# Optimization experiments

Measured on AMD Instinct MI355X. Metric: run time of the kernel, lower is better.

Reference implementation:

```python
import jax, jax.numpy as jnp
import numpy as np

N_NODES = 100000
HIDDEN = 128
N_LAYERS = 3
N_EDGES = 600000


def setup_inputs() -> dict:
    key = jax.random.key(0)
    k_e, k_emb, k_w = jax.random.split(key, 3)
    edge_index = jax.random.randint(k_e, (2, N_EDGES), 0, N_NODES, dtype=jnp.int64 if jax.config.read('jax_enable_x64') else jnp.int32)
    embedding = jax.random.normal(k_emb, (N_NODES, HIDDEN), dtype=jnp.float32)
    Ws = jax.random.normal(k_w, (N_LAYERS, HIDDEN, HIDDEN), dtype=jnp.float32) * (1.0 / np.sqrt(HIDDEN))
    bs = jnp.zeros((N_LAYERS, HIDDEN), dtype=jnp.float32)
    return {"edge_index": edge_index, "embedding": embedding, "Ws": Ws, "bs": bs}


def _gcn_forward(embedding, Ws, bs, edge_index):
    N = embedding.shape[0]
    # PyG GCNConv default: add self-loops, symmetric deg^{-1/2} normalization
    loop = jnp.arange(N, dtype=edge_index.dtype)
    src = jnp.concatenate([edge_index[0], loop])  # [E+N]
    dst = jnp.concatenate([edge_index[1], loop])
    deg = jax.ops.segment_sum(jnp.ones_like(dst, dtype=embedding.dtype), dst, num_segments=N)
    dinv = jnp.where(deg > 0, jax.lax.rsqrt(jnp.where(deg > 0, deg, 1.0)), 0.0)
    norm = dinv[src] * dinv[dst]  # [E+N]

    x = embedding
    for l in range(Ws.shape[0]):
        h = x @ Ws[l]                              # [N, d] linear transform
        msg = h[src] * norm[:, None]               # gather + scale
        x = jax.ops.segment_sum(msg, dst, num_segments=N) + bs[l]  # scatter-add
        x = jax.nn.relu(x)
        # dropout is identity in eval mode
    return x


def reference(edge_index, embedding, Ws, bs):
    return _gcn_forward(embedding, Ws, bs, edge_index)
```

## Files before the change

### kernel.cpp

```cpp
#include <hip/hip_runtime.h>
#include <hip/hip_bf16.h>


#define HID 128


__global__ void k_init_cnt(int* cnt, int n) {
    int i = blockIdx.x * blockDim.x + threadIdx.x;
    if (i < n) cnt[i] = 1;
}

__global__ void k_count_edges(const int* __restrict__ ei, int* cnt, int E) {
    int e = blockIdx.x * blockDim.x + threadIdx.x;
    if (e < E) atomicAdd(&cnt[ei[E + e]], 1);
}

__global__ void k_scanA(const int* __restrict__ cnt, int* csum, int n) {
    __shared__ int sd[256];
    int t = threadIdx.x;
    int base = blockIdx.x * 1024 + t * 4;
    int s = 0;
#pragma unroll
    for (int j = 0; j < 4; j++) { int i = base + j; if (i < n) s += cnt[i]; }
    sd[t] = s; __syncthreads();
    for (int off = 128; off > 0; off >>= 1) {
        if (t < off) sd[t] += sd[t + off];
        __syncthreads();
    }
    if (t == 0) csum[blockIdx.x] = sd[0];
}

__global__ void k_scanB(int* csum, int* offsets, int nchunk, int n) {
    __shared__ int sd[256];
    int t = threadIdx.x;
    int v = (t < nchunk) ? csum[t] : 0;
    sd[t] = v; __syncthreads();
    for (int off = 1; off < 256; off <<= 1) {
        int u = (t >= off) ? sd[t - off] : 0;
        __syncthreads();
        sd[t] += u;
        __syncthreads();
    }
    if (t < nchunk) csum[t] = sd[t] - v;
    if (t == 0) offsets[n] = sd[255];
}

__global__ void k_scanC(const int* __restrict__ cnt, const int* __restrict__ csum,
                        int* offsets, int* cursor, float* dinv,
                        int* adj_src, float* adj_norm, int n) {
    __shared__ int sd[256];
    int t = threadIdx.x;
    int base = blockIdx.x * 1024 + t * 4;
    int c[4]; int s = 0;
#pragma unroll
    for (int j = 0; j < 4; j++) {
        c[j] = (base + j < n) ? cnt[base + j] : 0;
        s += c[j];
    }
    sd[t] = s; __syncthreads();
    for (int off = 1; off < 256; off <<= 1) {
        int v = (t >= off) ? sd[t - off] : 0;
        __syncthreads();
        sd[t] += v;
        __syncthreads();
    }
    int run = sd[t] - s + csum[blockIdx.x];
#pragma unroll
    for (int j = 0; j < 4; j++) {
        int i = base + j;
        if (i < n) {
            offsets[i] = run;
            float di = rsqrtf((float)c[j]);
            dinv[i] = di;
            cursor[i] = run + 1;
            adj_src[run] = i;
            adj_norm[run] = di * di;
        }
        run += c[j];
    }
}

__global__ void k_fill_edges(const int* __restrict__ ei, int* cursor,
                             const float* __restrict__ dinv,
                             int* adj_src, float* adj_norm, int E) {
    int e = blockIdx.x * blockDim.x + threadIdx.x;
    if (e >= E) return;
    int s = ei[e];
    int d = ei[E + e];
    int pos = atomicAdd(&cursor[d], 1);
    adj_src[pos] = s;
    adj_norm[pos] = dinv[s] * dinv[d];
}


__global__ __launch_bounds__(256) void k_agg(const float* __restrict__ x,
                                             const int* __restrict__ offsets,
                                             const int* __restrict__ adj_src,
                                             const float* __restrict__ adj_norm,
                                             float* __restrict__ out, int n) {
    int gid = blockIdx.x * blockDim.x + threadIdx.x;
    int node = gid >> 6;
    int lane = gid & 63;
    if (node >= n) return;
    int beg = offsets[node];
    int end = offsets[node + 1];
    int q    = lane >> 4;
    int ql   = lane & 15;
    int f4   = (q & 1) * 16 + ql;
    int epar = q >> 1;
    float4 acc = {0.f, 0.f, 0.f, 0.f};
#pragma unroll 2
    for (int e = beg; e < end; e += 2) {
        int me = e + epar;
        int mc = me < end ? me : end - 1;
        int s  = adj_src[mc];
        float w = me < end ? adj_norm[mc] : 0.f;
        float4 v = ((const float4*)(x + (size_t)s * HID))[f4];
        acc.x += w * v.x;
        acc.y += w * v.y;
        acc.z += w * v.z;
        acc.w += w * v.w;
    }
    acc.x += __shfl_xor(acc.x, 32);
    acc.y += __shfl_xor(acc.y, 32);
    acc.z += __shfl_xor(acc.z, 32);
    acc.w += __shfl_xor(acc.w, 32);
    if (lane < 32)
        ((float4*)(out + (size_t)node * HID))[lane] = acc;
}


__global__ __launch_bounds__(256, 2) void k_gemm_bias_relu(const float* __restrict__ A,
                                                           const float* __restrict__ W,
                                                           const float* __restrict__ bias,
                                                           float* __restrict__ out,
                                                           int nrows) {
    __shared__ float Wl[HID * HID];
    __shared__ float Xs[32 * HID];
    int t = threadIdx.x;

    {
        const float4* Wg = (const float4*)W;
        float4* Wd = (float4*)Wl;
        for (int i = t; i < (HID * HID) / 4; i += 256) Wd[i] = Wg[i];
    }

    int tx = t & 31;
    int ty = t >> 5;
    int ntiles = nrows / 32;

    for (int tile = blockIdx.x; tile < ntiles; tile += gridDim.x) {
        __syncthreads();
        const float4* Ag = (const float4*)(A + (size_t)tile * 32 * HID);
        float4* Xd = (float4*)Xs;
#pragma unroll
        for (int i = 0; i < 4; i++) Xd[t + i * 256] = Ag[t + i * 256];
        __syncthreads();

        float acc[4][4] = {};
#pragma unroll 8
        for (int k = 0; k < HID; k++) {
            float4 wv = ((const float4*)(Wl + k * HID))[tx];
#pragma unroll
            for (int r = 0; r < 4; r++) {
                float xr = Xs[(ty * 4 + r) * HID + k];
                acc[r][0] += xr * wv.x;
                acc[r][1] += xr * wv.y;
                acc[r][2] += xr * wv.z;
                acc[r][3] += xr * wv.w;
            }
        }

        float4 bb = ((const float4*)bias)[tx];
#pragma unroll
        for (int r = 0; r < 4; r++) {
            float4 v;
            v.x = fmaxf(acc[r][0] + bb.x, 0.f);
            v.y = fmaxf(acc[r][1] + bb.y, 0.f);
            v.z = fmaxf(acc[r][2] + bb.z, 0.f);
            v.w = fmaxf(acc[r][3] + bb.w, 0.f);
            ((float4*)(out + (size_t)(tile * 32 + ty * 4 + r) * HID))[tx] = v;
        }
    }
}


extern "C" void kernel_launch(void* const* d_in, const int* in_sizes, int n_in,
                              void* d_out, int out_size, void* d_ws, size_t ws_size,
                              hipStream_t stream) {
    const int* ei = (const int*)d_in[0];
    const float* emb = (const float*)d_in[1];
    const float* Ws = (const float*)d_in[2];
    const float* bs = (const float*)d_in[3];

    const int E = in_sizes[0] / 2;
    const int N = in_sizes[1] / HID;
    const int NL = in_sizes[3] / HID;
    const int TOT = E + N;

    char* p = (char*)d_ws;
    auto carve = [&](size_t bytes) {
        char* r = p;
        p += (bytes + 255) & ~(size_t)255;
        return (void*)r;
    };
    int*   cnt      = (int*)  carve((size_t)N * 4);
    int*   offsets  = (int*)  carve((size_t)(N + 1) * 4);
    int*   cursor   = (int*)  carve((size_t)N * 4);
    float* dinv     = (float*)carve((size_t)N * 4);
    int*   csum     = (int*)  carve(1024 * 4);
    int*   adj_src  = (int*)  carve((size_t)TOT * 4);
    float* adj_norm = (float*)carve((size_t)TOT * 4);
    float* aggbuf   = (float*)carve((size_t)N * HID * 4);
    float* xbuf     = (float*)d_out;

    const int NCHUNK = (N + 1023) / 1024;

    k_init_cnt<<<(N + 255) / 256, 256, 0, stream>>>(cnt, N);
    k_count_edges<<<(E + 255) / 256, 256, 0, stream>>>(ei, cnt, E);
    k_scanA<<<NCHUNK, 256, 0, stream>>>(cnt, csum, N);
    k_scanB<<<1, 256, 0, stream>>>(csum, offsets, NCHUNK, N);
    k_scanC<<<NCHUNK, 256, 0, stream>>>(cnt, csum, offsets, cursor, dinv,
                                        adj_src, adj_norm, N);
    k_fill_edges<<<(E + 255) / 256, 256, 0, stream>>>(ei, cursor, dinv,
                                                      adj_src, adj_norm, E);

    const int aggBlocks = (N * 64 + 255) / 256;
    const float* x = emb;
    for (int l = 0; l < NL; l++) {
        k_agg<<<aggBlocks, 256, 0, stream>>>(x, offsets, adj_src, adj_norm, aggbuf, N);
        k_gemm_bias_relu<<<512, 256, 0, stream>>>(aggbuf, Ws + (size_t)l * HID * HID,
                                                  bs + (size_t)l * HID, xbuf, N);
        x = xbuf;
    }
}
```

Measured before the change: 502.5 us.

## Fuse neighbor aggregation with GEMM+bias+ReLU into one per-layer kernel

Each 512-thread block now gathers and normalizes the neighbor features for a 32-node tile directly into shared memory, then multiplies that tile by the LDS-resident weight matrix and applies bias and ReLU. This replaces the separate aggregation and GEMM kernels per layer and removes the full N×128 intermediate buffer write and re-read. Layer outputs ping-pong between a workspace buffer and the output. The trade-off is that the latency-bound gather now runs at the limited occupancy of a large-LDS persistent block, with the GEMM phase serialized behind it inside each block.

```diff
diff --git a/kernel.cpp b/kernel.cpp
--- a/kernel.cpp
+++ b/kernel.cpp
@@ -93,94 +93,83 @@
 }
 
 
-__global__ __launch_bounds__(256) void k_agg(const float* __restrict__ x,
-                                             const int* __restrict__ offsets,
-                                             const int* __restrict__ adj_src,
-                                             const float* __restrict__ adj_norm,
-                                             float* __restrict__ out, int n) {
-    int gid = blockIdx.x * blockDim.x + threadIdx.x;
-    int node = gid >> 6;
-    int lane = gid & 63;
-    if (node >= n) return;
-    int beg = offsets[node];
-    int end = offsets[node + 1];
+__global__ __launch_bounds__(512, 2) void k_layer(const float* __restrict__ x,
+                                                  const int* __restrict__ offsets,
+                                                  const int* __restrict__ adj_src,
+                                                  const float* __restrict__ adj_norm,
+                                                  const float* __restrict__ W,
+                                                  const float* __restrict__ bias,
+                                                  float* __restrict__ out, int n) {
+    __shared__ float Wl[HID * HID];
+    __shared__ float Xs[32 * HID];
+    int t = threadIdx.x;
+
+    {
+        const float4* Wg = (const float4*)W;
+        float4* Wd = (float4*)Wl;
+#pragma unroll
+        for (int i = 0; i < 8; i++) Wd[t + i * 512] = Wg[t + i * 512];
+    }
+
+    int wave = t >> 6;
+    int lane = t & 63;
     int q    = lane >> 4;
     int ql   = lane & 15;
     int f4   = (q & 1) * 16 + ql;
     int epar = q >> 1;
-    float4 acc = {0.f, 0.f, 0.f, 0.f};
-#pragma unroll 2
-    for (int e = beg; e < end; e += 2) {
-        int me = e + epar;
-        int mc = me < end ? me : end - 1;
-        int s  = adj_src[mc];
-        float w = me < end ? adj_norm[mc] : 0.f;
-        float4 v = ((const float4*)(x + (size_t)s * HID))[f4];
-        acc.x += w * v.x;
-        acc.y += w * v.y;
-        acc.z += w * v.z;
-        acc.w += w * v.w;
-    }
-    acc.x += __shfl_xor(acc.x, 32);
-    acc.y += __shfl_xor(acc.y, 32);
-    acc.z += __shfl_xor(acc.z, 32);
-    acc.w += __shfl_xor(acc.w, 32);
-    if (lane < 32)
-        ((float4*)(out + (size_t)node * HID))[lane] = acc;
-}
-
-
-__global__ __launch_bounds__(256, 2) void k_gemm_bias_relu(const float* __restrict__ A,
-                                                           const float* __restrict__ W,
-                                                           const float* __restrict__ bias,
-                                                           float* __restrict__ out,
-                                                           int nrows) {
-    __shared__ float Wl[HID * HID];
-    __shared__ float Xs[32 * HID];
-    int t = threadIdx.x;
-
-    {
-        const float4* Wg = (const float4*)W;
-        float4* Wd = (float4*)Wl;
-        for (int i = t; i < (HID * HID) / 4; i += 256) Wd[i] = Wg[i];
-    }
-
     int tx = t & 31;
     int ty = t >> 5;
-    int ntiles = nrows / 32;
+    int ntiles = n / 32;
 
     for (int tile = blockIdx.x; tile < ntiles; tile += gridDim.x) {
         __syncthreads();
-        const float4* Ag = (const float4*)(A + (size_t)tile * 32 * HID);
-        float4* Xd = (float4*)Xs;
-#pragma unroll
-        for (int i = 0; i < 4; i++) Xd[t + i * 256] = Ag[t + i * 256];
-        __syncthreads();
-
-        float acc[4][4] = {};
+
+        for (int i = 0; i < 4; i++) {
+            int r = wave * 4 + i;
+            int node = tile * 32 + r;
+            int beg = offsets[node];
+            int end = offsets[node + 1];
+            float4 acc = {0.f, 0.f, 0.f, 0.f};
+#pragma unroll 2
+            for (int e = beg; e < end; e += 2) {
+                int me = e + epar;
+                int mc = me < end ? me : end - 1;
+                int s  = adj_src[mc];
+                float w = me < end ? adj_norm[mc] : 0.f;
+                float4 v = ((const float4*)(x + (size_t)s * HID))[f4];
+                acc.x += w * v.x;
+                acc.y += w * v.y;
+                acc.z += w * v.z;
+                acc.w += w * v.w;
+            }
+            acc.x += __shfl_xor(acc.x, 32);
+            acc.y += __shfl_xor(acc.y, 32);
+            acc.z += __shfl_xor(acc.z, 32);
+            acc.w += __shfl_xor(acc.w, 32);
+            if (lane < 32)
+                ((float4*)(Xs + r * HID))[lane] = acc;
+        }
+        __syncthreads();
+
+        float a00 = 0.f, a01 = 0.f, a02 = 0.f, a03 = 0.f;
+        float a10 = 0.f, a11 = 0.f, a12 = 0.f, a13 = 0.f;
 #pragma unroll 8
         for (int k = 0; k < HID; k++) {
             float4 wv = ((const float4*)(Wl + k * HID))[tx];
-#pragma unroll
-            for (int r = 0; r < 4; r++) {
-                float xr = Xs[(ty * 4 + r) * HID + k];
-                acc[r][0] += xr * wv.x;
-                acc[r][1] += xr * wv.y;
-                acc[r][2] += xr * wv.z;
-                acc[r][3] += xr * wv.w;
-            }
+            float x0 = Xs[(ty * 2) * HID + k];
+            float x1 = Xs[(ty * 2 + 1) * HID + k];
+            a00 += x0 * wv.x; a01 += x0 * wv.y; a02 += x0 * wv.z; a03 += x0 * wv.w;
+            a10 += x1 * wv.x; a11 += x1 * wv.y; a12 += x1 * wv.z; a13 += x1 * wv.w;
         }
-
         float4 bb = ((const float4*)bias)[tx];
-#pragma unroll
-        for (int r = 0; r < 4; r++) {
-            float4 v;
-            v.x = fmaxf(acc[r][0] + bb.x, 0.f);
-            v.y = fmaxf(acc[r][1] + bb.y, 0.f);
-            v.z = fmaxf(acc[r][2] + bb.z, 0.f);
-            v.w = fmaxf(acc[r][3] + bb.w, 0.f);
-            ((float4*)(out + (size_t)(tile * 32 + ty * 4 + r) * HID))[tx] = v;
-        }
+        float4 o0, o1;
+        o0.x = fmaxf(a00 + bb.x, 0.f); o0.y = fmaxf(a01 + bb.y, 0.f);
+        o0.z = fmaxf(a02 + bb.z, 0.f); o0.w = fmaxf(a03 + bb.w, 0.f);
+        o1.x = fmaxf(a10 + bb.x, 0.f); o1.y = fmaxf(a11 + bb.y, 0.f);
+        o1.z = fmaxf(a12 + bb.z, 0.f); o1.w = fmaxf(a13 + bb.w, 0.f);
+        size_t row0 = (size_t)tile * 32 + ty * 2;
+        ((float4*)(out + row0 * HID))[tx] = o0;
+        ((float4*)(out + (row0 + 1) * HID))[tx] = o1;
     }
 }
 
@@ -211,8 +200,8 @@
     int*   csum     = (int*)  carve(1024 * 4);
     int*   adj_src  = (int*)  carve((size_t)TOT * 4);
     float* adj_norm = (float*)carve((size_t)TOT * 4);
-    float* aggbuf   = (float*)carve((size_t)N * HID * 4);
-    float* xbuf     = (float*)d_out;
+    float* xbufA    = (float*)carve((size_t)N * HID * 4);
+    float* xbufB    = (float*)d_out;
 
     const int NCHUNK = (N + 1023) / 1024;
 
@@ -225,12 +214,12 @@
     k_fill_edges<<<(E + 255) / 256, 256, 0, stream>>>(ei, cursor, dinv,
                                                       adj_src, adj_norm, E);
 
-    const int aggBlocks = (N * 64 + 255) / 256;
     const float* x = emb;
     for (int l = 0; l < NL; l++) {
-        k_agg<<<aggBlocks, 256, 0, stream>>>(x, offsets, adj_src, adj_norm, aggbuf, N);
-        k_gemm_bias_relu<<<512, 256, 0, stream>>>(aggbuf, Ws + (size_t)l * HID * HID,
-                                                  bs + (size_t)l * HID, xbuf, N);
-        x = xbuf;
-    }
-}
+        float* o = (l % 2 == 0) ? xbufB : xbufA;
+        k_layer<<<512, 512, 0, stream>>>(x, offsets, adj_src, adj_norm,
+                                         Ws + (size_t)l * HID * HID,
+                                         bs + (size_t)l * HID, o, N);
+        x = o;
+    }
+}
```

New measurement: 496.8 us. Within noise of the previous version (-1.2%).

## Use split-bf16 MFMA GEMM with agg emitting hi/lo bf16 pairs

Applied to the files above, without the earlier changes.

Replaces the scalar FP32 LDS-tiled GEMM with a matrix-core GEMM built on the bf16 16x16x32 MFMA. Both operands are split into hi and lo bf16 parts and combined with three MFMAs to approximate fp32 accuracy. The aggregation kernel now writes the hi/lo bf16 split directly, and a new kernel pre-packs the transposed weights into hi/lo form. This adds extra MFMA work and bf16 conversion cost. Accuracy is near fp32 but not exact, and the B fragments are read straight from global memory rather than LDS.

```diff
diff --git a/kernel.cpp b/kernel.cpp
--- a/kernel.cpp
+++ b/kernel.cpp
@@ -3,6 +3,9 @@
 
 
 #define HID 128
+
+typedef __attribute__((ext_vector_type(8))) short short8;
+typedef __attribute__((ext_vector_type(4))) float floatx4;
 
 
 __global__ void k_init_cnt(int* cnt, int n) {
@@ -92,12 +95,28 @@
     adj_norm[pos] = dinv[s] * dinv[d];
 }
 
+__global__ void k_packW(const float* __restrict__ Ws, ushort* Whp, ushort* Wlp,
+                        int nlayers) {
+    int idx = blockIdx.x * blockDim.x + threadIdx.x;
+    if (idx >= nlayers * HID * HID) return;
+    int l = idx >> 14;
+    int n = (idx >> 7) & 127;
+    int k = idx & 127;
+    float w = Ws[(size_t)l * HID * HID + k * HID + n];
+    __hip_bfloat16 hi = __float2bfloat16(w);
+    float lo = w - __bfloat162float(hi);
+    __hip_bfloat16 lo16 = __float2bfloat16(lo);
+    Whp[idx] = *(ushort*)&hi;
+    Wlp[idx] = *(ushort*)&lo16;
+}
+
 
 __global__ __launch_bounds__(256) void k_agg(const float* __restrict__ x,
                                              const int* __restrict__ offsets,
                                              const int* __restrict__ adj_src,
                                              const float* __restrict__ adj_norm,
-                                             float* __restrict__ out, int n) {
+                                             ushort* __restrict__ yh,
+                                             ushort* __restrict__ yl, int n) {
     int gid = blockIdx.x * blockDim.x + threadIdx.x;
     int node = gid >> 6;
     int lane = gid & 63;
@@ -125,61 +144,73 @@
     acc.y += __shfl_xor(acc.y, 32);
     acc.z += __shfl_xor(acc.z, 32);
     acc.w += __shfl_xor(acc.w, 32);
-    if (lane < 32)
-        ((float4*)(out + (size_t)node * HID))[lane] = acc;
-}
-
-
-__global__ __launch_bounds__(256, 2) void k_gemm_bias_relu(const float* __restrict__ A,
-                                                           const float* __restrict__ W,
-                                                           const float* __restrict__ bias,
-                                                           float* __restrict__ out,
-                                                           int nrows) {
-    __shared__ float Wl[HID * HID];
-    __shared__ float Xs[32 * HID];
-    int t = threadIdx.x;
-
-    {
-        const float4* Wg = (const float4*)W;
-        float4* Wd = (float4*)Wl;
-        for (int i = t; i < (HID * HID) / 4; i += 256) Wd[i] = Wg[i];
-    }
-
-    int tx = t & 31;
-    int ty = t >> 5;
-    int ntiles = nrows / 32;
-
-    for (int tile = blockIdx.x; tile < ntiles; tile += gridDim.x) {
-        __syncthreads();
-        const float4* Ag = (const float4*)(A + (size_t)tile * 32 * HID);
-        float4* Xd = (float4*)Xs;
-#pragma unroll
-        for (int i = 0; i < 4; i++) Xd[t + i * 256] = Ag[t + i * 256];
-        __syncthreads();
-
-        float acc[4][4] = {};
-#pragma unroll 8
-        for (int k = 0; k < HID; k++) {
-            float4 wv = ((const float4*)(Wl + k * HID))[tx];
-#pragma unroll
-            for (int r = 0; r < 4; r++) {
-                float xr = Xs[(ty * 4 + r) * HID + k];
-                acc[r][0] += xr * wv.x;
-                acc[r][1] += xr * wv.y;
-                acc[r][2] += xr * wv.z;
-                acc[r][3] += xr * wv.w;
+    if (lane < 32) {
+        float a[4] = {acc.x, acc.y, acc.z, acc.w};
+        ushort4 h, l;
+        ushort* hp = (ushort*)&h;
+        ushort* lp = (ushort*)&l;
+#pragma unroll
+        for (int j = 0; j < 4; j++) {
+            __hip_bfloat16 hi = __float2bfloat16(a[j]);
+            float lo = a[j] - __bfloat162float(hi);
+            __hip_bfloat16 lo16 = __float2bfloat16(lo);
+            hp[j] = *(ushort*)&hi;
+            lp[j] = *(ushort*)&lo16;
+        }
+        ((ushort4*)(yh + (size_t)node * HID))[lane] = h;
+        ((ushort4*)(yl + (size_t)node * HID))[lane] = l;
+    }
+}
+
+
+__global__ __launch_bounds__(256) void k_gemm_mfma(const ushort* __restrict__ yh,
+                                                   const ushort* __restrict__ yl,
+                                                   const ushort* __restrict__ Whp,
+                                                   const ushort* __restrict__ Wlp,
+                                                   const float* __restrict__ bias,
+                                                   float* __restrict__ out, int n) {
+    int t = threadIdx.x;
+    int wave = t >> 6;
+    int lane = t & 63;
+    int m16  = lane & 15;
+    int oct  = lane >> 4;
+
+    int rowA = blockIdx.x * 64 + wave * 16 + m16;
+    const ushort* ah_base = yh + (size_t)rowA * HID + oct * 8;
+    const ushort* al_base = yl + (size_t)rowA * HID + oct * 8;
+
+    floatx4 acc[8];
+#pragma unroll
+    for (int c = 0; c < 8; c++) acc[c] = (floatx4){0.f, 0.f, 0.f, 0.f};
+
+#pragma unroll
+    for (int ks = 0; ks < 4; ks++) {
+        short8 ah = *(const short8*)(ah_base + ks * 32);
+        short8 al = *(const short8*)(al_base + ks * 32);
+#pragma unroll
+        for (int c = 0; c < 8; c++) {
+            const ushort* bp = Whp + (size_t)(c * 16 + m16) * HID + ks * 32 + oct * 8;
+            const ushort* bq = Wlp + (size_t)(c * 16 + m16) * HID + ks * 32 + oct * 8;
+            short8 bh = *(const short8*)bp;
+            short8 bl = *(const short8*)bq;
+            acc[c] = __builtin_amdgcn_mfma_f32_16x16x32_bf16(ah, bh, acc[c], 0, 0, 0);
+            acc[c] = __builtin_amdgcn_mfma_f32_16x16x32_bf16(ah, bl, acc[c], 0, 0, 0);
+            acc[c] = __builtin_amdgcn_mfma_f32_16x16x32_bf16(al, bh, acc[c], 0, 0, 0);
+        }
+    }
+
+    int rowbase = blockIdx.x * 64 + wave * 16 + oct * 4;
+#pragma unroll
+    for (int c = 0; c < 8; c++) {
+        int col = c * 16 + m16;
+        float b = bias[col];
+#pragma unroll
+        for (int r = 0; r < 4; r++) {
+            int row = rowbase + r;
+            if (row < n) {
+                float v = fmaxf(acc[c][r] + b, 0.f);
+                out[(size_t)row * HID + col] = v;
             }
-        }
-
-        float4 bb = ((const float4*)bias)[tx];
-#pragma unroll
-        for (int r = 0; r < 4; r++) {
-            float4 v;
-            v.x = fmaxf(acc[r][0] + bb.x, 0.f);
-            v.y = fmaxf(acc[r][1] + bb.y, 0.f);
-            v.z = fmaxf(acc[r][2] + bb.z, 0.f);
-            v.w = fmaxf(acc[r][3] + bb.w, 0.f);
-            ((float4*)(out + (size_t)(tile * 32 + ty * 4 + r) * HID))[tx] = v;
         }
     }
 }
@@ -197,6 +228,7 @@
     const int N = in_sizes[1] / HID;
     const int NL = in_sizes[3] / HID;
     const int TOT = E + N;
+    const int NPAD = ((N + 63) / 64) * 64;
 
     char* p = (char*)d_ws;
     auto carve = [&](size_t bytes) {
@@ -204,15 +236,19 @@
         p += (bytes + 255) & ~(size_t)255;
         return (void*)r;
     };
-    int*   cnt      = (int*)  carve((size_t)N * 4);
-    int*   offsets  = (int*)  carve((size_t)(N + 1) * 4);
-    int*   cursor   = (int*)  carve((size_t)N * 4);
-    float* dinv     = (float*)carve((size_t)N * 4);
-    int*   csum     = (int*)  carve(1024 * 4);
-    int*   adj_src  = (int*)  carve((size_t)TOT * 4);
-    float* adj_norm = (float*)carve((size_t)TOT * 4);
-    float* aggbuf   = (float*)carve((size_t)N * HID * 4);
-    float* xbuf     = (float*)d_out;
+    int*    cnt      = (int*)   carve((size_t)N * 4);
+    int*    offsets  = (int*)   carve((size_t)(N + 1) * 4);
+    int*    cursor   = (int*)   carve((size_t)N * 4);
+    float*  dinv     = (float*) carve((size_t)N * 4);
+    int*    csum     = (int*)   carve(1024 * 4);
+    int*    adj_src  = (int*)   carve((size_t)TOT * 4);
+    float*  adj_norm = (float*) carve((size_t)TOT * 4);
+    ushort* yh       = (ushort*)carve((size_t)NPAD * HID * 2);
+    ushort* yl       = (ushort*)carve((size_t)NPAD * HID * 2);
+    ushort* Whp      = (ushort*)carve((size_t)NL * HID * HID * 2);
+    ushort* Wlp      = (ushort*)carve((size_t)NL * HID * HID * 2);
+    float*  xbufA    = (float*) carve((size_t)N * HID * 4);
+    float*  xbufB    = (float*) d_out;
 
     const int NCHUNK = (N + 1023) / 1024;
 
@@ -224,13 +260,18 @@
                                         adj_src, adj_norm, N);
     k_fill_edges<<<(E + 255) / 256, 256, 0, stream>>>(ei, cursor, dinv,
                                                       adj_src, adj_norm, E);
+    k_packW<<<(NL * HID * HID + 255) / 256, 256, 0, stream>>>(Ws, Whp, Wlp, NL);
 
     const int aggBlocks = (N * 64 + 255) / 256;
+    const int gemmBlocks = NPAD / 64;
     const float* x = emb;
     for (int l = 0; l < NL; l++) {
-        k_agg<<<aggBlocks, 256, 0, stream>>>(x, offsets, adj_src, adj_norm, aggbuf, N);
-        k_gemm_bias_relu<<<512, 256, 0, stream>>>(aggbuf, Ws + (size_t)l * HID * HID,
-                                                  bs + (size_t)l * HID, xbuf, N);
-        x = xbuf;
-    }
-}
+        float* o = (l == 1) ? xbufA : xbufB;
+        k_agg<<<aggBlocks, 256, 0, stream>>>(x, offsets, adj_src, adj_norm, yh, yl, N);
+        k_gemm_mfma<<<gemmBlocks, 256, 0, stream>>>(yh, yl,
+                                                    Whp + (size_t)l * HID * HID,
+                                                    Wlp + (size_t)l * HID * HID,
+                                                    bs + (size_t)l * HID, o, N);
+        x = o;
+    }
+}
```

New measurement: 547.2 us. 8.9% more time.
